# Optimization experiments

Hardware: AMD Instinct MI355X
Metric: run time of the kernel (lower is better)

The kernel has to match this reference:

```python
import jax, jax.numpy as jnp
import numpy as np

NUM_HEADS = 10
LN_EPS = 1e-5


def setup_inputs() -> dict:
    key = jax.random.key(0)
    ks = jax.random.split(key, 6)
    N, D = 4096, 640  # in_dim == out_dim required by residual add
    x = jax.random.normal(ks[0], (N, D), dtype=jnp.float32)
    s = 1.0 / np.sqrt(D)
    Wq = jax.random.normal(ks[1], (D, D), dtype=jnp.float32) * s  # torch Linear weight [out,in]
    Wk = jax.random.normal(ks[2], (D, D), dtype=jnp.float32) * s
    Wv = jax.random.normal(ks[3], (D, D), dtype=jnp.float32) * s
    gamma = jnp.ones((D,), dtype=jnp.float32)
    beta = jnp.zeros((D,), dtype=jnp.float32)
    return {"x": x, "Wq": Wq, "Wk": Wk, "Wv": Wv, "gamma": gamma, "beta": beta}


def reference(x, Wq, Wk, Wv, gamma, beta):
    N, D = x.shape
    dk = D // NUM_HEADS
    Q = x @ Wq.T  # [N, D]
    K = x @ Wk.T
    V = x @ Wv.T
    # Faithful to source: raw reshapes (NOT transposes)
    Qh = Q.reshape(NUM_HEADS, N, dk)
    Kh = K.reshape(NUM_HEADS, N, dk).reshape(NUM_HEADS, dk, N)  # torch.reshape, not .mT
    Vh = V.reshape(NUM_HEADS, N, dk)
    # Faithful quirk: scale by sqrt(K.shape[2]) == sqrt(N)
    scale = np.float32(np.sqrt(N))
    wghts = jax.nn.softmax((Qh @ Kh) / scale, axis=-1)  # [H, N, N]
    values = wghts @ Vh  # [H, N, dk]
    values = values.reshape(N, NUM_HEADS * dk)  # raw reshape merge
    values = values + x  # residual
    # LayerNorm(out_dim), biased variance, eps=1e-5
    mean = jnp.mean(values, axis=-1, keepdims=True)
    var = jnp.mean(jnp.square(values - mean), axis=-1, keepdims=True)
    out = (values - mean) * jax.lax.rsqrt(var + LN_EPS) * gamma + beta
    return out
```

## Files before the change

kernel.cpp:

```cpp
#include <hip/hip_runtime.h>
#if __has_include(<hip/hip_fp8.h>)
#include <hip/hip_fp8.h>
#endif


typedef __bf16 bf16x8 __attribute__((ext_vector_type(8)));
typedef __bf16 bf16x4 __attribute__((ext_vector_type(4)));
typedef float  f32x4  __attribute__((ext_vector_type(4)));
typedef unsigned short u16x4 __attribute__((ext_vector_type(4)));
typedef unsigned int   u32x4 __attribute__((ext_vector_type(4)));
typedef long           lx2   __attribute__((ext_vector_type(2)));
typedef lx2            lx2a  __attribute__((may_alias));
typedef long           la64  __attribute__((may_alias));
typedef unsigned int   ua32  __attribute__((may_alias));

#define N_TOK   4096
#define D_MODEL 640
#define DK      64
#define HSLAB   (N_TOK * DK)
#define SQS 0.15014030f

#if __has_builtin(__builtin_amdgcn_exp2f)
#define EXP2(x) __builtin_amdgcn_exp2f(x)
#else
#define EXP2(x) exp2f(x)
#endif

__device__ __forceinline__ void stage16(const void* g, void* lds_uniform) {
    __builtin_amdgcn_global_load_lds(
        (const __attribute__((address_space(1))) unsigned int*)g,
        (__attribute__((address_space(3))) unsigned int*)lds_uniform, 16, 0, 0);
}

__device__ __forceinline__ u16x4 cvt4(f32x4 v) {
    return __builtin_bit_cast(u16x4, __builtin_convertvector(v, bf16x4));
}

__device__ __forceinline__ unsigned int pk_fp8(f32x4 v) {
#if __has_builtin(__builtin_amdgcn_cvt_pk_fp8_f32)
    int r = 0;
    r = __builtin_amdgcn_cvt_pk_fp8_f32(v[0], v[1], r, false);
    r = __builtin_amdgcn_cvt_pk_fp8_f32(v[2], v[3], r, true);
    return (unsigned int)r;
#else
    union { unsigned char b[4]; unsigned int u; } x;
    x.b[0] = __hip_fp8_e4m3(v[0]).__x;
    x.b[1] = __hip_fp8_e4m3(v[1]).__x;
    x.b[2] = __hip_fp8_e4m3(v[2]).__x;
    x.b[3] = __hip_fp8_e4m3(v[3]).__x;
    return x.u;
#endif
}

__global__ __launch_bounds__(256) void cvt_all(const float* __restrict__ x,
                                               const float* __restrict__ w0,
                                               const float* __restrict__ w1,
                                               const float* __restrict__ w2,
                                               unsigned short* __restrict__ xb,
                                               unsigned short* __restrict__ d0,
                                               unsigned short* __restrict__ d1,
                                               unsigned short* __restrict__ d2,
                                               f32x4* __restrict__ ltot4) {
    int i = blockIdx.x * 256 + threadIdx.x;
    if (i >= 962560) { ltot4[i - 962560] = (f32x4){0.f, 0.f, 0.f, 0.f}; return; }
    const float* s; unsigned short* d; int off; float scl = 1.0f;
    if (i < 655360) { s = x; d = xb; off = i; }
    else {
        int j = i - 655360;
        int w = j / 102400; off = j - w * 102400;
        s = (w == 0) ? w0 : (w == 1) ? w1 : w2;
        d = (w == 0) ? d0 : (w == 1) ? d1 : d2;
        if (w < 2) scl = SQS;
    }
    f32x4 v = ((const f32x4*)s)[off];
    v[0] *= scl; v[1] *= scl; v[2] *= scl; v[3] *= scl;
    ((u16x4*)d)[off] = cvt4(v);
}

__global__ __launch_bounds__(256, 2) void gemm_qkv(
    const unsigned short* __restrict__ xb,
    const unsigned short* __restrict__ wq,
    const unsigned short* __restrict__ wk,
    const unsigned short* __restrict__ wv,
    unsigned char*  __restrict__ Qf8o,
    unsigned short* __restrict__ Ko,
    unsigned short* __restrict__ Vo) {
    const int b = blockIdx.x;
    const int g = b & 31;
    const int r = b >> 5;
    const int mode = r / 5;
    const int m0 = g * 128;
    const int n0 = (r % 5) * 128;
    const unsigned short* W = (mode == 0) ? wq : (mode == 1) ? wk : wv;
    unsigned short*       C = (mode == 1) ? Ko : Vo;

    __shared__ unsigned short As[8192];
    __shared__ unsigned short Bs[8192];

    const int tid  = threadIdx.x;
    const int lane = tid & 63;
    const int wave = tid >> 6;
    const int quad = lane >> 4, l16 = lane & 15;
    const int wm = (wave >> 1) * 64, wn = (wave & 1) * 64;
    const int swz = l16 & 7;

    f32x4 acc[4][4] = {};

    int prow[4], pcol[4], lbase[4];
    for (int j = 0; j < 4; j++) {
        int p = j * 256 + tid;
        prow[j] = p >> 3;
        pcol[j] = ((p & 7) ^ (prow[j] & 7)) * 8;
        lbase[j] = (j * 256 + wave * 64) * 8;
    }

    for (int kt = 0; kt < D_MODEL; kt += 64) {
        __syncthreads();
        for (int j = 0; j < 4; j++) {
            stage16(&xb[(size_t)(m0 + prow[j]) * D_MODEL + kt + pcol[j]], As + lbase[j]);
            stage16(&W [(size_t)(n0 + prow[j]) * D_MODEL + kt + pcol[j]], Bs + lbase[j]);
        }
        __syncthreads();

        for (int s = 0; s < 2; s++) {
            bf16x8 af[4], bfr[4];
            for (int mi = 0; mi < 4; mi++) {
                int row = wm + mi * 16 + l16;
                af[mi] = *(const bf16x8*)&As[row * 64 + (((s << 2) + quad) ^ swz) * 8];
            }
            for (int ni = 0; ni < 4; ni++) {
                int row = wn + ni * 16 + l16;
                bfr[ni] = *(const bf16x8*)&Bs[row * 64 + (((s << 2) + quad) ^ swz) * 8];
            }
            for (int mi = 0; mi < 4; mi++)
                for (int ni = 0; ni < 4; ni++)
                    acc[mi][ni] = __builtin_amdgcn_mfma_f32_16x16x32_bf16(af[mi], bfr[ni], acc[mi][ni], 0, 0, 0);
        }
    }

    if (mode == 0) {
        for (int mi = 0; mi < 4; mi++)
            for (int ni = 0; ni < 4; ni++) {
                unsigned int p = pk_fp8(acc[mi][ni]);
                for (int r2 = 0; r2 < 4; r2++) {
                    int row = m0 + wm + mi * 16 + quad * 4 + r2;
                    int col = n0 + wn + ni * 16 + l16;
                    Qf8o[(size_t)row * D_MODEL + col] = (unsigned char)(p >> (r2 * 8));
                }
            }
    } else {
        for (int mi = 0; mi < 4; mi++)
            for (int ni = 0; ni < 4; ni++) {
                u16x4 cv = cvt4(acc[mi][ni]);
                for (int r2 = 0; r2 < 4; r2++) {
                    int row = m0 + wm + mi * 16 + quad * 4 + r2;
                    int col = n0 + wn + ni * 16 + l16;
                    C[(size_t)row * D_MODEL + col] = cv[r2];
                }
            }
    }
}

__global__ __launch_bounds__(256) void transpose_kv(
    const unsigned short* __restrict__ Kn, unsigned char* __restrict__ Kp8,
    const unsigned short* __restrict__ Vn, unsigned char* __restrict__ Vp8) {
    const int z = blockIdx.z;
    const int t = threadIdx.x;

    __shared__ unsigned short T[64][66];
    const unsigned short* src; unsigned char* dst;
    int R, Cc, r0, c0;
    if (z < 10) { src = Kn; dst = Kp8; R = 64;   Cc = 4096; r0 = 0; c0 = blockIdx.x * 64; }
    else        { src = Vn; dst = Vp8; R = 4096; Cc = 64;   r0 = blockIdx.x * 64; c0 = 0; }
    const size_t hb = (size_t)(z % 10) * HSLAB;
    const int rr = t >> 3, c8 = (t & 7) * 8;
    const int pbase = ((c8 & 31) >> 3) * 16 + (c8 >> 5) * 8;

    for (int hf = 0; hf < 2; hf++) {
        int r = rr + hf * 32;
        bf16x8 v = *(const bf16x8*)&src[hb + (size_t)(r0 + r) * Cc + c0 + c8];
        for (int j = 0; j < 8; j++) T[r][c8 + j] = ((unsigned short*)&v)[j];
    }
    __syncthreads();
    const bf16x8 zz = {};
    for (int hf = 0; hf < 2; hf++) {
        int r = rr + hf * 32;
        *(bf16x8*)&((unsigned short*)src)[hb + (size_t)(r0 + r) * Cc + c0 + c8] = zz;
    }
    for (int hf = 0; hf < 2; hf++) {
        int oc = rr + hf * 32;
        f32x4 lo, hi;
        for (int j = 0; j < 4; j++) {
            lo[j] = __builtin_bit_cast(float, (unsigned int)T[c8 + j][oc] << 16);
            hi[j] = __builtin_bit_cast(float, (unsigned int)T[c8 + 4 + j][oc] << 16);
        }
        uint2 ov; ov.x = pk_fp8(lo); ov.y = pk_fp8(hi);
        size_t dcol = (z < 10) ? ((size_t)(c0 + oc) * 64 + pbase)
                               : ((size_t)oc * 4096 + r0 + pbase);
        *(uint2*)&dst[hb + dcol] = ov;
    }
}

__global__ __launch_bounds__(256, 4) void attn(
    const unsigned char* __restrict__ Qf8,
    const unsigned char* __restrict__ Kp8,
    const unsigned char* __restrict__ Vp8,
    float* __restrict__ vals,
    float* __restrict__ l_tot) {
    const int h  = blockIdx.x >> 5;
    const int qt = blockIdx.x & 31;
    const int ntile = (blockIdx.y == 2) ? 10 : 11;
    const int tile0 = blockIdx.y * 11;
    const int lane = threadIdx.x & 63;
    const int wave = threadIdx.x >> 6;
    const int quad = lane >> 4, l16 = lane & 15;
    const size_t hoff = (size_t)h * HSLAB;

    __shared__ unsigned char sm[40960];
    unsigned char* const Kb0 = sm;
    unsigned char* const Kb1 = sm + 8192;
    unsigned char* const Vt  = sm + 16384;
    unsigned char* const Pw  = sm + 24576 + wave * 4096;

    const int qbase = qt * 128 + wave * 32;
    long qd[2][2];
    for (int g = 0; g < 2; g++) {
        const unsigned char* qp = Qf8 + hoff + (size_t)(qbase + g * 16 + l16) * 64 + quad * 8;
        qd[g][0] = *(const la64*)(qp);
        qd[g][1] = *(const la64*)(qp + 32);
    }

    f32x4 o[2][4] = {};
    f32x4 ol[2] = {};
    const long ONES8 = 0x3838383838383838L;

    const int cA = wave * 64 + lane, cB = cA + 256;
    const int vDA = cA >> 3, vSA = ((cA & 7) * 16) ^ ((vDA & 7) << 4);
    const int vDB = cB >> 3, vSB = ((cB & 7) * 16) ^ ((vDB & 7) << 4);

    const int kfb = l16 * 64 + quad * 16;
    const int vrb = l16 * 128;
    const int vx  = (l16 & 7) << 4;

    {
        const size_t kb0 = hoff + (size_t)(tile0 << 7) * 64;
        stage16(Kp8 + kb0 + cA * 16, Kb0 + wave * 1024);
        stage16(Kp8 + kb0 + cB * 16, Kb0 + 4096 + wave * 1024);
    }

    for (int t = 0; t < ntile; t++) {
        const int keyb = (tile0 + t) << 7;
        unsigned char* const Kcur = (t & 1) ? Kb1 : Kb0;

        __syncthreads();

        if (t + 1 < ntile) {
            const size_t kbn = hoff + (size_t)((tile0 + t + 1) << 7) * 64;
            unsigned char* const Knext = (t & 1) ? Kb0 : Kb1;
            stage16(Kp8 + kbn + cA * 16, Knext + wave * 1024);
            stage16(Kp8 + kbn + cB * 16, Knext + 4096 + wave * 1024);
        }
        stage16(Vp8 + hoff + (size_t)vDA * N_TOK + keyb + vSA, Vt + wave * 1024);
        stage16(Vp8 + hoff + (size_t)vDB * N_TOK + keyb + vSB, Vt + 4096 + wave * 1024);

        for (int ni = 0; ni < 8; ni++) {
            lx2 kk = *(const lx2a*)(Kcur + ni * 1024 + kfb);
            for (int g = 0; g < 2; g++) {
                f32x4 s = {};
                s = __builtin_amdgcn_mfma_f32_16x16x32_fp8_fp8(kk[0], qd[g][0], s, 0, 0, 0);
                s = __builtin_amdgcn_mfma_f32_16x16x32_fp8_fp8(kk[1], qd[g][1], s, 0, 0, 0);
                f32x4 pv;
                for (int r = 0; r < 4; r++) pv[r] = EXP2(s[r]);
                const int pu = ni * 2 + (quad >> 1);
                *(ua32*)(Pw + pu * 256 +
                         (((g * 16 + l16) + ((pu & 3) << 3)) & 31) * 8 +
                         (quad & 1) * 4) = pk_fp8(pv);
            }
        }

        __syncthreads();

        for (int ksp = 0; ksp < 2; ksp++) {
            lx2 vv[4];
            for (int nd = 0; nd < 4; nd++)
                vv[nd] = *(const lx2a*)(Vt + nd * 2048 + vrb +
                                        ((ksp * 64 + quad * 16) ^ vx));
            for (int kh = 0; kh < 2; kh++) {
                const int ks = ksp * 2 + kh;
                for (int g = 0; g < 2; g++) {
                    long pf = *(const la64*)(Pw + (ks * 4 + quad) * 256 +
                                             (((g * 16 + l16) + (quad << 3)) & 31) * 8);
                    ol[g] = __builtin_amdgcn_mfma_f32_16x16x32_fp8_fp8(pf, ONES8, ol[g], 0, 0, 0);
                    for (int nd = 0; nd < 4; nd++)
                        o[g][nd] = __builtin_amdgcn_mfma_f32_16x16x32_fp8_fp8(pf, vv[nd][kh], o[g][nd], 0, 0, 0);
                }
            }
        }
    }

    if (l16 == 0)
        for (int g = 0; g < 2; g++)
            for (int r = 0; r < 4; r++)
                atomicAdd(&l_tot[(h << 12) + qbase + g * 16 + quad * 4 + r], ol[g][r]);

    for (int g = 0; g < 2; g++)
        for (int nd = 0; nd < 4; nd++)
            for (int r = 0; r < 4; r++) {
                int q = qbase + g * 16 + quad * 4 + r;
                atomicAdd(&vals[hoff + (size_t)q * DK + nd * 16 + l16], o[g][nd][r]);
            }
}

__global__ __launch_bounds__(256) void ln_kernel(
    const float* __restrict__ vals, const float* __restrict__ l_tot,
    const float* __restrict__ x,
    const float* __restrict__ gamma, const float* __restrict__ beta,
    float* __restrict__ out) {
    const int wave = threadIdx.x >> 6, lane = threadIdx.x & 63;
    const int row  = blockIdx.x * 4 + wave;
    const float* v  = vals + (size_t)row * D_MODEL;
    const float* xr = x    + (size_t)row * D_MODEL;

    float t[10];
    float s = 0.f;
    for (int i = 0; i < 10; i++) {
        float linv = 1.0f / l_tot[row * 10 + i];
        t[i] = v[lane + i * 64] * linv + xr[lane + i * 64];
        s += t[i];
    }
    for (int off = 32; off; off >>= 1) s += __shfl_xor(s, off, 64);
    float mean = s * (1.0f / 640.0f);
    float s2 = 0.f;
    for (int i = 0; i < 10; i++) { float d = t[i] - mean; s2 += d * d; }
    for (int off = 32; off; off >>= 1) s2 += __shfl_xor(s2, off, 64);
    float inv = rsqrtf(s2 * (1.0f / 640.0f) + 1e-5f);

    float* orow = out + (size_t)row * D_MODEL;
    for (int i = 0; i < 10; i++) {
        int c = lane + i * 64;
        orow[c] = (t[i] - mean) * inv * gamma[c] + beta[c];
    }
}

extern "C" void kernel_launch(void* const* d_in, const int* in_sizes, int n_in,
                              void* d_out, int out_size, void* d_ws, size_t ws_size,
                              hipStream_t stream) {
    const float* x     = (const float*)d_in[0];
    const float* Wq    = (const float*)d_in[1];
    const float* Wk    = (const float*)d_in[2];
    const float* Wv    = (const float*)d_in[3];
    const float* gamma = (const float*)d_in[4];
    const float* beta  = (const float*)d_in[5];
    float* out = (float*)d_out;

    char* ws = (char*)d_ws;
    unsigned short* xb  = (unsigned short*)(ws);
    unsigned short* wqb = (unsigned short*)(ws + 5242880);
    unsigned short* wkb = (unsigned short*)(ws + 6062080);
    unsigned short* wvb = (unsigned short*)(ws + 6881280);
    unsigned char*  Qf8 = (unsigned char*)(ws + 7700480);
    unsigned char*  Kp8 = (unsigned char*)(ws + 12943360);
    unsigned char*  Vp8 = (unsigned char*)(ws + 18186240);
    unsigned short* Kn  = (unsigned short*)(ws + 23429120);
    unsigned short* Vn  = (unsigned short*)(ws + 28672000);
    float*          vals  = (float*)(ws + 23429120);
    float*          l_tot = (float*)(ws + 33914880);

    cvt_all<<<3800, 256, 0, stream>>>(x, Wq, Wk, Wv, xb, wqb, wkb, wvb,
                                      (f32x4*)l_tot);

    gemm_qkv<<<480, 256, 0, stream>>>(xb, wqb, wkb, wvb, Qf8, Kn, Vn);

    transpose_kv<<<dim3(64, 1, 20), 256, 0, stream>>>(Kn, Kp8, Vn, Vp8);

    attn<<<dim3(320, 3), 256, 0, stream>>>(Qf8, Kp8, Vp8, vals, l_tot);
    ln_kernel<<<1024, 256, 0, stream>>>(vals, l_tot, x, gamma, beta, out);
}
```

Baseline: 149.6 us.

## Fuse LayerNorm into attention kernel via last-arriving-block counters

Removes the separate LayerNorm launch. Per-row-group atomic counters, reset in transpose_kv, let the last of the 30 attention blocks contributing to a 128-row slab apply normalization, residual and LayerNorm to that slab. This saves a kernel launch and lets normalization overlap with attention blocks still running. The cost is that only 32 blocks do all of LayerNorm, each wave looping over 32 rows in sequence, which can leave a latency-bound tail at the end of the attention kernel.

```diff
diff --git a/kernel.cpp b/kernel.cpp
--- a/kernel.cpp
+++ b/kernel.cpp
@@ -163,9 +163,12 @@
 
 __global__ __launch_bounds__(256) void transpose_kv(
     const unsigned short* __restrict__ Kn, unsigned char* __restrict__ Kp8,
-    const unsigned short* __restrict__ Vn, unsigned char* __restrict__ Vp8) {
+    const unsigned short* __restrict__ Vn, unsigned char* __restrict__ Vp8,
+    int* __restrict__ cnt) {
     const int z = blockIdx.z;
     const int t = threadIdx.x;
+
+    if (z == 0 && blockIdx.x == 0 && t < 32) cnt[t] = 0;
 
     __shared__ unsigned short T[64][66];
     const unsigned short* src; unsigned char* dst;
@@ -206,7 +209,12 @@
     const unsigned char* __restrict__ Kp8,
     const unsigned char* __restrict__ Vp8,
     float* __restrict__ vals,
-    float* __restrict__ l_tot) {
+    float* __restrict__ l_tot,
+    int* __restrict__ cnt,
+    const float* __restrict__ xg,
+    const float* __restrict__ gamma,
+    const float* __restrict__ beta,
+    float* __restrict__ out) {
     const int h  = blockIdx.x >> 5;
     const int qt = blockIdx.x & 31;
     const int ntile = (blockIdx.y == 2) ? 10 : 11;
@@ -309,36 +317,42 @@
                 int q = qbase + g * 16 + quad * 4 + r;
                 atomicAdd(&vals[hoff + (size_t)q * DK + nd * 16 + l16], o[g][nd][r]);
             }
-}
-
-__global__ __launch_bounds__(256) void ln_kernel(
-    const float* __restrict__ vals, const float* __restrict__ l_tot,
-    const float* __restrict__ x,
-    const float* __restrict__ gamma, const float* __restrict__ beta,
-    float* __restrict__ out) {
-    const int wave = threadIdx.x >> 6, lane = threadIdx.x & 63;
-    const int row  = blockIdx.x * 4 + wave;
-    const float* v  = vals + (size_t)row * D_MODEL;
-    const float* xr = x    + (size_t)row * D_MODEL;
-
-    float t[10];
-    float s = 0.f;
-    for (int i = 0; i < 10; i++) {
-        float linv = 1.0f / l_tot[row * 10 + i];
-        t[i] = v[lane + i * 64] * linv + xr[lane + i * 64];
-        s += t[i];
-    }
-    for (int off = 32; off; off >>= 1) s += __shfl_xor(s, off, 64);
-    float mean = s * (1.0f / 640.0f);
-    float s2 = 0.f;
-    for (int i = 0; i < 10; i++) { float d = t[i] - mean; s2 += d * d; }
-    for (int off = 32; off; off >>= 1) s2 += __shfl_xor(s2, off, 64);
-    float inv = rsqrtf(s2 * (1.0f / 640.0f) + 1e-5f);
-
-    float* orow = out + (size_t)row * D_MODEL;
-    for (int i = 0; i < 10; i++) {
-        int c = lane + i * 64;
-        orow[c] = (t[i] - mean) * inv * gamma[c] + beta[c];
+
+    __threadfence();
+    __syncthreads();
+    int* const lastf = (int*)sm;
+    if (threadIdx.x == 0) {
+        const int R = blockIdx.x / 10;
+        lastf[0] = (atomicAdd(&cnt[R], 1) == 29) ? 1 : 0;
+    }
+    __syncthreads();
+    if (!lastf[0]) return;
+    __threadfence();
+
+    const int r0 = (blockIdx.x / 10) * 128 + wave * 32;
+    for (int w = 0; w < 32; w++) {
+        const int row = r0 + w;
+        const float* v  = vals + (size_t)row * D_MODEL;
+        const float* xr = xg   + (size_t)row * D_MODEL;
+        float tt[10];
+        float s = 0.f;
+        for (int i = 0; i < 10; i++) {
+            float linv = 1.0f / l_tot[row * 10 + i];
+            tt[i] = v[lane + i * 64] * linv + xr[lane + i * 64];
+            s += tt[i];
+        }
+        for (int off = 32; off; off >>= 1) s += __shfl_xor(s, off, 64);
+        float mean = s * (1.0f / 640.0f);
+        float s2 = 0.f;
+        for (int i = 0; i < 10; i++) { float d = tt[i] - mean; s2 += d * d; }
+        for (int off = 32; off; off >>= 1) s2 += __shfl_xor(s2, off, 64);
+        float inv = rsqrtf(s2 * (1.0f / 640.0f) + 1e-5f);
+
+        float* orow = out + (size_t)row * D_MODEL;
+        for (int i = 0; i < 10; i++) {
+            int c = lane + i * 64;
+            orow[c] = (tt[i] - mean) * inv * gamma[c] + beta[c];
+        }
     }
 }
 
@@ -365,14 +379,15 @@
     unsigned short* Vn  = (unsigned short*)(ws + 28672000);
     float*          vals  = (float*)(ws + 23429120);
     float*          l_tot = (float*)(ws + 33914880);
+    int*            cnt   = (int*)(ws + 34078720);
 
     cvt_all<<<3800, 256, 0, stream>>>(x, Wq, Wk, Wv, xb, wqb, wkb, wvb,
                                       (f32x4*)l_tot);
 
     gemm_qkv<<<480, 256, 0, stream>>>(xb, wqb, wkb, wvb, Qf8, Kn, Vn);
 
-    transpose_kv<<<dim3(64, 1, 20), 256, 0, stream>>>(Kn, Kp8, Vn, Vp8);
-
-    attn<<<dim3(320, 3), 256, 0, stream>>>(Qf8, Kp8, Vp8, vals, l_tot);
-    ln_kernel<<<1024, 256, 0, stream>>>(vals, l_tot, x, gamma, beta, out);
-}
+    transpose_kv<<<dim3(64, 1, 20), 256, 0, stream>>>(Kn, Kp8, Vn, Vp8, cnt);
+
+    attn<<<dim3(320, 3), 256, 0, stream>>>(Qf8, Kp8, Vp8, vals, l_tot, cnt,
+                                           x, gamma, beta, out);
+}
```

Measured after the change: 265.6 us. 1.78x slower.

## Shrink attention query tile to 16 rows per wave and split keys in halves

Applied to the files above, without the earlier changes.

The attention kernel now gives each wave 16 query rows instead of 32, so a block covers 64 queries, and it splits the 32 key tiles into two halves of 16 instead of three uneven chunks. The grid becomes 640x2 blocks and the per-wave P scratch in shared memory halves, which lowers LDS and register use per block. The intent is to raise occupancy and balance work across the blocks. The cost is that each K/V tile staged into shared memory is reused by half as many queries, so K/V load traffic per unit of compute roughly doubles.

```diff
diff --git a/kernel.cpp b/kernel.cpp
--- a/kernel.cpp
+++ b/kernel.cpp
@@ -207,31 +207,30 @@
     const unsigned char* __restrict__ Vp8,
     float* __restrict__ vals,
     float* __restrict__ l_tot) {
-    const int h  = blockIdx.x >> 5;
-    const int qt = blockIdx.x & 31;
-    const int ntile = (blockIdx.y == 2) ? 10 : 11;
-    const int tile0 = blockIdx.y * 11;
+    const int h  = blockIdx.x >> 6;
+    const int qt = blockIdx.x & 63;
+    const int tile0 = blockIdx.y * 16;
     const int lane = threadIdx.x & 63;
     const int wave = threadIdx.x >> 6;
     const int quad = lane >> 4, l16 = lane & 15;
     const size_t hoff = (size_t)h * HSLAB;
 
-    __shared__ unsigned char sm[40960];
+    __shared__ unsigned char sm[32768];
     unsigned char* const Kb0 = sm;
     unsigned char* const Kb1 = sm + 8192;
     unsigned char* const Vt  = sm + 16384;
-    unsigned char* const Pw  = sm + 24576 + wave * 4096;
-
-    const int qbase = qt * 128 + wave * 32;
-    long qd[2][2];
-    for (int g = 0; g < 2; g++) {
-        const unsigned char* qp = Qf8 + hoff + (size_t)(qbase + g * 16 + l16) * 64 + quad * 8;
-        qd[g][0] = *(const la64*)(qp);
-        qd[g][1] = *(const la64*)(qp + 32);
-    }
-
-    f32x4 o[2][4] = {};
-    f32x4 ol[2] = {};
+    unsigned char* const Pw  = sm + 24576 + wave * 2048;
+
+    const int qbase = qt * 64 + wave * 16;
+    long qd0, qd1;
+    {
+        const unsigned char* qp = Qf8 + hoff + (size_t)(qbase + l16) * 64 + quad * 8;
+        qd0 = *(const la64*)(qp);
+        qd1 = *(const la64*)(qp + 32);
+    }
+
+    f32x4 o[4] = {};
+    f32x4 ol = {};
     const long ONES8 = 0x3838383838383838L;
 
     const int cA = wave * 64 + lane, cB = cA + 256;
@@ -248,13 +247,13 @@
         stage16(Kp8 + kb0 + cB * 16, Kb0 + 4096 + wave * 1024);
     }
 
-    for (int t = 0; t < ntile; t++) {
+    for (int t = 0; t < 16; t++) {
         const int keyb = (tile0 + t) << 7;
         unsigned char* const Kcur = (t & 1) ? Kb1 : Kb0;
 
         __syncthreads();
 
-        if (t + 1 < ntile) {
+        if (t + 1 < 16) {
             const size_t kbn = hoff + (size_t)((tile0 + t + 1) << 7) * 64;
             unsigned char* const Knext = (t & 1) ? Kb0 : Kb1;
             stage16(Kp8 + kbn + cA * 16, Knext + wave * 1024);
@@ -265,17 +264,15 @@
 
         for (int ni = 0; ni < 8; ni++) {
             lx2 kk = *(const lx2a*)(Kcur + ni * 1024 + kfb);
-            for (int g = 0; g < 2; g++) {
-                f32x4 s = {};
-                s = __builtin_amdgcn_mfma_f32_16x16x32_fp8_fp8(kk[0], qd[g][0], s, 0, 0, 0);
-                s = __builtin_amdgcn_mfma_f32_16x16x32_fp8_fp8(kk[1], qd[g][1], s, 0, 0, 0);
-                f32x4 pv;
-                for (int r = 0; r < 4; r++) pv[r] = EXP2(s[r]);
-                const int pu = ni * 2 + (quad >> 1);
-                *(ua32*)(Pw + pu * 256 +
-                         (((g * 16 + l16) + ((pu & 3) << 3)) & 31) * 8 +
-                         (quad & 1) * 4) = pk_fp8(pv);
-            }
+            f32x4 s = {};
+            s = __builtin_amdgcn_mfma_f32_16x16x32_fp8_fp8(kk[0], qd0, s, 0, 0, 0);
+            s = __builtin_amdgcn_mfma_f32_16x16x32_fp8_fp8(kk[1], qd1, s, 0, 0, 0);
+            f32x4 pv;
+            for (int r = 0; r < 4; r++) pv[r] = EXP2(s[r]);
+            const int pu = ni * 2 + (quad >> 1);
+            *(ua32*)(Pw + pu * 128 +
+                     ((l16 + ((pu & 1) << 3)) & 15) * 8 +
+                     (quad & 1) * 4) = pk_fp8(pv);
         }
 
         __syncthreads();
@@ -287,28 +284,24 @@
                                         ((ksp * 64 + quad * 16) ^ vx));
             for (int kh = 0; kh < 2; kh++) {
                 const int ks = ksp * 2 + kh;
-                for (int g = 0; g < 2; g++) {
-                    long pf = *(const la64*)(Pw + (ks * 4 + quad) * 256 +
-                                             (((g * 16 + l16) + (quad << 3)) & 31) * 8);
-                    ol[g] = __builtin_amdgcn_mfma_f32_16x16x32_fp8_fp8(pf, ONES8, ol[g], 0, 0, 0);
-                    for (int nd = 0; nd < 4; nd++)
-                        o[g][nd] = __builtin_amdgcn_mfma_f32_16x16x32_fp8_fp8(pf, vv[nd][kh], o[g][nd], 0, 0, 0);
-                }
+                long pf = *(const la64*)(Pw + (ks * 4 + quad) * 128 +
+                                         ((l16 + ((quad & 1) << 3)) & 15) * 8);
+                ol = __builtin_amdgcn_mfma_f32_16x16x32_fp8_fp8(pf, ONES8, ol, 0, 0, 0);
+                for (int nd = 0; nd < 4; nd++)
+                    o[nd] = __builtin_amdgcn_mfma_f32_16x16x32_fp8_fp8(pf, vv[nd][kh], o[nd], 0, 0, 0);
             }
         }
     }
 
     if (l16 == 0)
-        for (int g = 0; g < 2; g++)
-            for (int r = 0; r < 4; r++)
-                atomicAdd(&l_tot[(h << 12) + qbase + g * 16 + quad * 4 + r], ol[g][r]);
-
-    for (int g = 0; g < 2; g++)
-        for (int nd = 0; nd < 4; nd++)
-            for (int r = 0; r < 4; r++) {
-                int q = qbase + g * 16 + quad * 4 + r;
-                atomicAdd(&vals[hoff + (size_t)q * DK + nd * 16 + l16], o[g][nd][r]);
-            }
+        for (int r = 0; r < 4; r++)
+            atomicAdd(&l_tot[(h << 12) + qbase + quad * 4 + r], ol[r]);
+
+    for (int nd = 0; nd < 4; nd++)
+        for (int r = 0; r < 4; r++) {
+            int q = qbase + quad * 4 + r;
+            atomicAdd(&vals[hoff + (size_t)q * DK + nd * 16 + l16], o[nd][r]);
+        }
 }
 
 __global__ __launch_bounds__(256) void ln_kernel(
@@ -373,6 +366,6 @@
 
     transpose_kv<<<dim3(64, 1, 20), 256, 0, stream>>>(Kn, Kp8, Vn, Vp8);
 
-    attn<<<dim3(320, 3), 256, 0, stream>>>(Qf8, Kp8, Vp8, vals, l_tot);
+    attn<<<dim3(640, 2), 256, 0, stream>>>(Qf8, Kp8, Vp8, vals, l_tot);
     ln_kernel<<<1024, 256, 0, stream>>>(vals, l_tot, x, gamma, beta, out);
 }
```

Result: no change. 150.7 us (+0.7%).
